# Performance work log

Hardware: AMD Instinct MI355X
Metric: run time of the kernel (lower is better)

Reference implementation:

```python
import jax, jax.numpy as jnp
import numpy as np

N_NODES = 100000
N_EDGES = 1600000
IN_F = 256
OUT_F = 128


def setup_inputs() -> dict:
    key = jax.random.key(0)
    k1, k2, k3, k4, k5, k6 = jax.random.split(key, 6)
    x = jax.random.normal(k1, (N_NODES, IN_F), dtype=jnp.float32)
    edge_row = jax.random.randint(k2, (N_EDGES,), 0, N_NODES)  # destination (output row)
    edge_col = jax.random.randint(k3, (N_EDGES,), 0, N_NODES)  # source (gathered node)
    edge_val = jax.random.uniform(k4, (N_EDGES,), dtype=jnp.float32)  # normalized adj weights
    # Xavier-uniform init like nn.init.xavier_uniform_
    limit = float(np.sqrt(6.0 / (IN_F + OUT_F)))
    weight = jax.random.uniform(k5, (IN_F, OUT_F), dtype=jnp.float32, minval=-limit, maxval=limit)
    bias = jnp.zeros((OUT_F,), dtype=jnp.float32)
    return {"x": x, "edge_row": edge_row, "edge_col": edge_col,
            "edge_val": edge_val, "weight": weight, "bias": bias}


def reference(x, edge_row, edge_col, edge_val, weight, bias):
    # Dense transform: h = x @ W + b   -> [N, OUT_F]
    h = x @ weight + bias
    # Sparse adjacency matmul: out[i] = sum_{e: row[e]==i} val[e] * h[col[e]]
    msg = h[edge_col] * edge_val[:, None]  # [E, OUT_F] gather + scale
    out = jax.ops.segment_sum(msg, edge_row, num_segments=N_NODES)
    return out
```

## Files before the change

kernel.cpp:

```cpp
#include <hip/hip_runtime.h>

#define IN_F 256
#define OUT_F 128

typedef __attribute__((ext_vector_type(8))) short short8;
typedef __attribute__((ext_vector_type(4))) float floatx4;

__device__ __forceinline__ unsigned short f2bf(float f) {
    union { float f; unsigned int u; } v; v.f = f;
    unsigned int u = v.u;
    unsigned int r = (u + 0x7FFFu + ((u >> 16) & 1u)) >> 16;
    return (unsigned short)r;
}

__global__ __launch_bounds__(256) void prep_kernel(
    const float* __restrict__ w, unsigned short* __restrict__ w_t,
    int* __restrict__ ghist, int nb)
{
    const int g = blockIdx.x * 256 + threadIdx.x;
    if (g < IN_F * OUT_F) {
        const int n = g >> 8;
        const int k = g & 255;
        w_t[n * 256 + k] = f2bf(w[k * OUT_F + n]);
    }
    const int z = g - IN_F * OUT_F;
    if (z >= 0 && z < nb) ghist[z] = 0;
}

#define XS2 264
#define HS2 136

__global__ __launch_bounds__(256) void gemm_mfma_kernel(
    const float* __restrict__ x, const unsigned short* __restrict__ w_t,
    const float* __restrict__ bias, unsigned short* __restrict__ h_bf, int M)
{
    __shared__ unsigned short xs[64 * XS2];

    const int tid  = threadIdx.x;
    const int w    = tid >> 6;
    const int l    = tid & 63;
    const int m16  = l & 15;
    const int g    = l >> 4;
    const int row0 = blockIdx.x * 64;

    short8 bf[2][8];
    #pragma unroll
    for (int nt = 0; nt < 2; nt++)
        #pragma unroll
        for (int ks = 0; ks < 8; ks++)
            bf[nt][ks] = *(const short8*)(
                w_t + (w * 32 + nt * 16 + m16) * 256 + ks * 32 + g * 8);

    #pragma unroll
    for (int s = 0; s < 16; s++) {
        const int idx = tid + s * 256;
        const int row = idx >> 6;
        const int c4  = idx & 63;
        const int gr  = row0 + row;
        float4 v = make_float4(0.f, 0.f, 0.f, 0.f);
        if (gr < M) v = *(const float4*)(x + (size_t)gr * IN_F + c4 * 4);
        ushort4 b;
        b.x = f2bf(v.x); b.y = f2bf(v.y); b.z = f2bf(v.z); b.w = f2bf(v.w);
        *(ushort4*)(xs + row * XS2 + c4 * 4) = b;
    }
    __syncthreads();

    floatx4 acc[4][2];
    #pragma unroll
    for (int mt = 0; mt < 4; mt++) {
        acc[mt][0] = (floatx4){0.f, 0.f, 0.f, 0.f};
        acc[mt][1] = (floatx4){0.f, 0.f, 0.f, 0.f};
    }

    #pragma unroll
    for (int ks = 0; ks < 8; ks++) {
        #pragma unroll
        for (int mt = 0; mt < 4; mt++) {
            const short8 a = *(const short8*)(xs + (mt * 16 + m16) * XS2 + ks * 32 + g * 8);
            acc[mt][0] = __builtin_amdgcn_mfma_f32_16x16x32_bf16(a, bf[0][ks], acc[mt][0], 0, 0, 0);
            acc[mt][1] = __builtin_amdgcn_mfma_f32_16x16x32_bf16(a, bf[1][ks], acc[mt][1], 0, 0, 0);
        }
    }
    __syncthreads();

    unsigned short* hs = xs;
    #pragma unroll
    for (int nt = 0; nt < 2; nt++) {
        const int col = w * 32 + nt * 16 + m16;
        const float bv = bias[col];
        #pragma unroll
        for (int mt = 0; mt < 4; mt++)
            #pragma unroll
            for (int r = 0; r < 4; r++)
                hs[(mt * 16 + g * 4 + r) * HS2 + col] = f2bf(acc[mt][nt][r] + bv);
    }
    __syncthreads();

    {
        const int row = tid >> 2;
        const int seg = tid & 3;
        const int gr  = row0 + row;
        if (gr < M) {
            #pragma unroll
            for (int q = 0; q < 4; q++) {
                const uint4 v = *(const uint4*)(hs + row * HS2 + seg * 32 + q * 8);
                *(uint4*)(h_bf + (size_t)gr * OUT_F + seg * 32 + q * 8) = v;
            }
        }
    }
}


__global__ __launch_bounds__(256) void hist_kernel(
    const int* __restrict__ erow, int* __restrict__ ghist, int E, int nb)
{
    __shared__ int lh[512];
    for (int i = threadIdx.x; i < nb; i += 256) lh[i] = 0;
    __syncthreads();
    const int base = blockIdx.x * 8192;
    for (int i = 0; i < 32; i++) {
        const int e = base + i * 256 + threadIdx.x;
        if (e < E) atomicAdd(&lh[erow[e] >> 8], 1);
    }
    __syncthreads();
    for (int i = threadIdx.x; i < nb; i += 256)
        if (lh[i]) atomicAdd(&ghist[i], lh[i]);
}

__global__ __launch_bounds__(512) void scanb_kernel(
    const int* __restrict__ ghist, int* __restrict__ bucketStart,
    int* __restrict__ cursor, int nb, int M, int E, int* __restrict__ start)
{
    __shared__ int sd[512];
    const int t = threadIdx.x;
    const int v = (t < nb) ? ghist[t] : 0;
    sd[t] = v;
    __syncthreads();
    for (int off = 1; off < 512; off <<= 1) {
        const int u = (t >= off) ? sd[t - off] : 0;
        __syncthreads();
        sd[t] += u;
        __syncthreads();
    }
    if (t < nb) { const int ex = sd[t] - v; bucketStart[t] = ex; cursor[t] = ex; }
    if (t == 0) { bucketStart[nb] = E; start[M] = E; }
}

__global__ __launch_bounds__(256) void sort_kernel(
    const int* __restrict__ erow, const int* __restrict__ ecol,
    const float* __restrict__ eval, int* __restrict__ cursor,
    uint2* __restrict__ tmp, int E, int nb)
{
    __shared__ int lcnt[512], lbase[512];
    for (int i = threadIdx.x; i < nb; i += 256) lcnt[i] = 0;
    __syncthreads();
    const int base = blockIdx.x * 8192;
    for (int i = 0; i < 32; i++) {
        const int e = base + i * 256 + threadIdx.x;
        if (e < E) atomicAdd(&lcnt[erow[e] >> 8], 1);
    }
    __syncthreads();
    for (int i = threadIdx.x; i < nb; i += 256) {
        const int c = lcnt[i];
        lbase[i] = c ? atomicAdd(&cursor[i], c) : 0;
        lcnt[i] = 0;
    }
    __syncthreads();
    for (int i = 0; i < 32; i++) {
        const int e = base + i * 256 + threadIdx.x;
        if (e < E) {
            const int r = erow[e];
            const int b = r >> 8;
            const int lp = atomicAdd(&lcnt[b], 1);
            tmp[lbase[b] + lp] = make_uint2(
                ((unsigned int)(r & 255) << 24) | (unsigned int)ecol[e],
                __float_as_uint(eval[e]));
        }
    }
}

__global__ __launch_bounds__(256) void csr_kernel(
    const uint2* __restrict__ tmp, const int* __restrict__ bucketStart,
    int* __restrict__ start, unsigned int* __restrict__ cv, int M)
{
    __shared__ int nh[256], nst[256], ncur[256];
    __shared__ unsigned int lcv[8192];
    const int b  = blockIdx.x;
    const int s0 = bucketStart[b];
    const int s1 = bucketStart[b + 1];
    const int cnt = min(s1 - s0, 8192);
    const int t  = threadIdx.x;

    nh[t] = 0;
    __syncthreads();
    for (int i = t; i < cnt; i += 256) atomicAdd(&nh[tmp[s0 + i].x >> 24], 1);
    __syncthreads();

    const int v = nh[t];
    nst[t] = v;
    __syncthreads();
    for (int off = 1; off < 256; off <<= 1) {
        const int u = (t >= off) ? nst[t - off] : 0;
        __syncthreads();
        nst[t] += u;
        __syncthreads();
    }
    const int ex = nst[t] - v;
    const int node = b * 256 + t;
    if (node < M) start[node] = s0 + ex;
    ncur[t] = ex;
    __syncthreads();

    for (int i = t; i < cnt; i += 256) {
        const uint2 p = tmp[s0 + i];
        const int d  = p.x >> 24;
        const int lp = atomicAdd(&ncur[d], 1);
        const float f = __uint_as_float(p.y);
        const int q = min((int)(f * 32768.0f), 32767);
        lcv[lp] = ((p.x & 0x00FFFFFFu) << 15) | (unsigned int)q;
    }
    __syncthreads();
    for (int i = t; i < cnt; i += 256) cv[s0 + i] = lcv[i];
}

__global__ __launch_bounds__(256) void gather_kernel(
    const unsigned short* __restrict__ h_bf, const int* __restrict__ start,
    const unsigned int* __restrict__ cv, float* __restrict__ out, int N)
{
    const int node = (blockIdx.x * 256 + threadIdx.x) >> 6;
    const int lane = threadIdx.x & 63;
    if (node >= N) return;

    const int s   = start[node];
    const int end = start[node + 1];
    const unsigned int* hp = (const unsigned int*)h_bf;

    float acc0 = 0.f, acc1 = 0.f;
    int j = s;
    for (; j + 8 <= end; j += 8) {
        unsigned int mu[8];
        const unsigned int* rp[8];
        #pragma unroll
        for (int u = 0; u < 8; u++) {
            mu[u] = __builtin_amdgcn_readfirstlane(cv[j + u]);
            rp[u] = hp + (size_t)(mu[u] >> 15) * 64;
        }
        unsigned int p[8];
        #pragma unroll
        for (int u = 0; u < 8; u++) p[u] = rp[u][lane];
        #pragma unroll
        for (int u = 0; u < 8; u++) {
            const float v = (float)(mu[u] & 0x7FFFu) * (1.0f / 32768.0f) + (0.5f / 32768.0f);
            acc0 += v * __uint_as_float(p[u] << 16);
            acc1 += v * __uint_as_float(p[u] & 0xFFFF0000u);
        }
    }
    for (; j < end; j++) {
        const unsigned int mu = __builtin_amdgcn_readfirstlane(cv[j]);
        const unsigned int p = *(hp + (size_t)(mu >> 15) * 64 + lane);
        const float v = (float)(mu & 0x7FFFu) * (1.0f / 32768.0f) + (0.5f / 32768.0f);
        acc0 += v * __uint_as_float(p << 16);
        acc1 += v * __uint_as_float(p & 0xFFFF0000u);
    }
    float2 o; o.x = acc0; o.y = acc1;
    *(float2*)(out + (size_t)node * OUT_F + lane * 2) = o;
}

extern "C" void kernel_launch(void* const* d_in, const int* in_sizes, int n_in,
                              void* d_out, int out_size, void* d_ws, size_t ws_size,
                              hipStream_t stream) {
    const float* x     = (const float*)d_in[0];
    const int*   erow  = (const int*)d_in[1];
    const int*   ecol  = (const int*)d_in[2];
    const float* eval  = (const float*)d_in[3];
    const float* wgt   = (const float*)d_in[4];
    const float* bias  = (const float*)d_in[5];
    float*       out   = (float*)d_out;

    const int M  = in_sizes[0] / IN_F;
    const int E  = in_sizes[1];
    const int nb = (M + 255) >> 8;
    const int EB = (E + 8191) / 8192;

    char* ws = (char*)d_ws;
    unsigned short* h_bf = (unsigned short*)ws;  ws += (size_t)M * OUT_F * 2;
    unsigned short* w_t  = (unsigned short*)ws;  ws += (size_t)IN_F * OUT_F * 2;
    int* ghist       = (int*)ws;                 ws += ((size_t)nb * 4 + 15) & ~15ull;
    int* bucketStart = (int*)ws;                 ws += ((size_t)(nb + 1) * 4 + 15) & ~15ull;
    int* cursor      = (int*)ws;                 ws += ((size_t)nb * 4 + 15) & ~15ull;
    int* start       = (int*)ws;                 ws += ((size_t)(M + 1) * 4 + 15) & ~15ull;
    uint2* tmp       = (uint2*)ws;               ws += (size_t)E * 8;
    unsigned int* cv = (unsigned int*)ws;        ws += (size_t)E * 4;

    prep_kernel<<<(IN_F * OUT_F + nb + 255) / 256, 256, 0, stream>>>(wgt, w_t, ghist, nb);
    gemm_mfma_kernel<<<(M + 63) / 64, 256, 0, stream>>>(x, w_t, bias, h_bf, M);

    hist_kernel<<<EB, 256, 0, stream>>>(erow, ghist, E, nb);
    scanb_kernel<<<1, 512, 0, stream>>>(ghist, bucketStart, cursor, nb, M, E, start);
    sort_kernel<<<EB, 256, 0, stream>>>(erow, ecol, eval, cursor, tmp, E, nb);
    csr_kernel<<<nb, 256, 0, stream>>>(tmp, bucketStart, start, cv, M);

    const long long work = (long long)M * 64;
    gather_kernel<<<(int)((work + 255) / 256), 256, 0, stream>>>(
        h_bf, start, cv, out, M);
}
```

Measured before the change: 339.1 us.

## Split GEMM tiles across hist, sort and CSR kernels to overlap work

The dense GEMM is split into three tile ranges, and each range is fused as extra blocks into the histogram, sort and CSR-build kernels via blockIdx dispatch with shared smem buffers. This lets the compute-bound GEMM run alongside the latency- and atomic-bound CSR construction stages, filling idle CUs and removing the standalone GEMM launch. The cost is that each fused kernel now reserves the larger shared-memory footprint for every block, which can lower occupancy for the small hist and sort blocks. GEMM tiles can also end up scheduled unevenly behind those blocks.

```diff
diff --git a/kernel.cpp b/kernel.cpp
--- a/kernel.cpp
+++ b/kernel.cpp
@@ -29,19 +29,23 @@
 
 #define XS2 264
 #define HS2 136
-
-__global__ __launch_bounds__(256) void gemm_mfma_kernel(
+#define GEMM_SMEM 33792
+#define CSR_SMEM  35840
+
+__device__ __forceinline__ void gemm_body(
+    char* smem,
     const float* __restrict__ x, const unsigned short* __restrict__ w_t,
-    const float* __restrict__ bias, unsigned short* __restrict__ h_bf, int M)
-{
-    __shared__ unsigned short xs[64 * XS2];
+    const float* __restrict__ bias, unsigned short* __restrict__ h_bf,
+    int tile, int M)
+{
+    unsigned short* xs = (unsigned short*)smem;
 
     const int tid  = threadIdx.x;
     const int w    = tid >> 6;
     const int l    = tid & 63;
     const int m16  = l & 15;
     const int g    = l >> 4;
-    const int row0 = blockIdx.x * 64;
+    const int row0 = tile * 64;
 
     short8 bf[2][8];
     #pragma unroll
@@ -110,14 +114,14 @@
     }
 }
 
-
-__global__ __launch_bounds__(256) void hist_kernel(
-    const int* __restrict__ erow, int* __restrict__ ghist, int E, int nb)
-{
-    __shared__ int lh[512];
+__device__ __forceinline__ void hist_body(
+    char* smem, const int* __restrict__ erow, int* __restrict__ ghist,
+    int E, int nb, int blk)
+{
+    int* lh = (int*)smem;
     for (int i = threadIdx.x; i < nb; i += 256) lh[i] = 0;
     __syncthreads();
-    const int base = blockIdx.x * 8192;
+    const int base = blk * 8192;
     for (int i = 0; i < 32; i++) {
         const int e = base + i * 256 + threadIdx.x;
         if (e < E) atomicAdd(&lh[erow[e] >> 8], 1);
@@ -127,34 +131,16 @@
         if (lh[i]) atomicAdd(&ghist[i], lh[i]);
 }
 
-__global__ __launch_bounds__(512) void scanb_kernel(
-    const int* __restrict__ ghist, int* __restrict__ bucketStart,
-    int* __restrict__ cursor, int nb, int M, int E, int* __restrict__ start)
-{
-    __shared__ int sd[512];
-    const int t = threadIdx.x;
-    const int v = (t < nb) ? ghist[t] : 0;
-    sd[t] = v;
-    __syncthreads();
-    for (int off = 1; off < 512; off <<= 1) {
-        const int u = (t >= off) ? sd[t - off] : 0;
-        __syncthreads();
-        sd[t] += u;
-        __syncthreads();
-    }
-    if (t < nb) { const int ex = sd[t] - v; bucketStart[t] = ex; cursor[t] = ex; }
-    if (t == 0) { bucketStart[nb] = E; start[M] = E; }
-}
-
-__global__ __launch_bounds__(256) void sort_kernel(
-    const int* __restrict__ erow, const int* __restrict__ ecol,
+__device__ __forceinline__ void sort_body(
+    char* smem, const int* __restrict__ erow, const int* __restrict__ ecol,
     const float* __restrict__ eval, int* __restrict__ cursor,
-    uint2* __restrict__ tmp, int E, int nb)
-{
-    __shared__ int lcnt[512], lbase[512];
+    uint2* __restrict__ tmp, int E, int nb, int blk)
+{
+    int* lcnt  = (int*)smem;
+    int* lbase = lcnt + 512;
     for (int i = threadIdx.x; i < nb; i += 256) lcnt[i] = 0;
     __syncthreads();
-    const int base = blockIdx.x * 8192;
+    const int base = blk * 8192;
     for (int i = 0; i < 32; i++) {
         const int e = base + i * 256 + threadIdx.x;
         if (e < E) atomicAdd(&lcnt[erow[e] >> 8], 1);
@@ -179,13 +165,16 @@
     }
 }
 
-__global__ __launch_bounds__(256) void csr_kernel(
-    const uint2* __restrict__ tmp, const int* __restrict__ bucketStart,
-    int* __restrict__ start, unsigned int* __restrict__ cv, int M)
-{
-    __shared__ int nh[256], nst[256], ncur[256];
-    __shared__ unsigned int lcv[8192];
-    const int b  = blockIdx.x;
+__device__ __forceinline__ void csr_body(
+    char* smem, const uint2* __restrict__ tmp, const int* __restrict__ bucketStart,
+    int* __restrict__ start, unsigned int* __restrict__ cv, int M, int blk)
+{
+    int* nh   = (int*)smem;
+    int* nst  = nh + 256;
+    int* ncur = nst + 256;
+    unsigned int* lcv = (unsigned int*)(smem + 3072);
+
+    const int b  = blk;
     const int s0 = bucketStart[b];
     const int s1 = bucketStart[b + 1];
     const int cnt = min(s1 - s0, 8192);
@@ -221,6 +210,67 @@
     }
     __syncthreads();
     for (int i = t; i < cnt; i += 256) cv[s0 + i] = lcv[i];
+}
+
+__global__ __launch_bounds__(256) void k_hist_gemm(
+    const int* __restrict__ erow, int* __restrict__ ghist, int E, int nb, int EB,
+    const float* __restrict__ x, const unsigned short* __restrict__ w_t,
+    const float* __restrict__ bias, unsigned short* __restrict__ h_bf,
+    int M, int tile0)
+{
+    __shared__ __align__(16) char smem[GEMM_SMEM];
+    if ((int)blockIdx.x < EB)
+        hist_body(smem, erow, ghist, E, nb, blockIdx.x);
+    else
+        gemm_body(smem, x, w_t, bias, h_bf, tile0 + (int)blockIdx.x - EB, M);
+}
+
+__global__ __launch_bounds__(256) void k_sort_gemm(
+    const int* __restrict__ erow, const int* __restrict__ ecol,
+    const float* __restrict__ eval, int* __restrict__ cursor,
+    uint2* __restrict__ tmp, int E, int nb, int EB,
+    const float* __restrict__ x, const unsigned short* __restrict__ w_t,
+    const float* __restrict__ bias, unsigned short* __restrict__ h_bf,
+    int M, int tile0)
+{
+    __shared__ __align__(16) char smem[GEMM_SMEM];
+    if ((int)blockIdx.x < EB)
+        sort_body(smem, erow, ecol, eval, cursor, tmp, E, nb, blockIdx.x);
+    else
+        gemm_body(smem, x, w_t, bias, h_bf, tile0 + (int)blockIdx.x - EB, M);
+}
+
+__global__ __launch_bounds__(256) void k_csr_gemm(
+    const uint2* __restrict__ tmp, const int* __restrict__ bucketStart,
+    int* __restrict__ start, unsigned int* __restrict__ cv, int nb,
+    const float* __restrict__ x, const unsigned short* __restrict__ w_t,
+    const float* __restrict__ bias, unsigned short* __restrict__ h_bf,
+    int M, int tile0)
+{
+    __shared__ __align__(16) char smem[CSR_SMEM];
+    if ((int)blockIdx.x < nb)
+        csr_body(smem, tmp, bucketStart, start, cv, M, blockIdx.x);
+    else
+        gemm_body(smem, x, w_t, bias, h_bf, tile0 + (int)blockIdx.x - nb, M);
+}
+
+__global__ __launch_bounds__(512) void scanb_kernel(
+    const int* __restrict__ ghist, int* __restrict__ bucketStart,
+    int* __restrict__ cursor, int nb, int M, int E, int* __restrict__ start)
+{
+    __shared__ int sd[512];
+    const int t = threadIdx.x;
+    const int v = (t < nb) ? ghist[t] : 0;
+    sd[t] = v;
+    __syncthreads();
+    for (int off = 1; off < 512; off <<= 1) {
+        const int u = (t >= off) ? sd[t - off] : 0;
+        __syncthreads();
+        sd[t] += u;
+        __syncthreads();
+    }
+    if (t < nb) { const int ex = sd[t] - v; bucketStart[t] = ex; cursor[t] = ex; }
+    if (t == 0) { bucketStart[nb] = E; start[M] = E; }
 }
 
 __global__ __launch_bounds__(256) void gather_kernel(
@@ -281,6 +331,9 @@
     const int E  = in_sizes[1];
     const int nb = (M + 255) >> 8;
     const int EB = (E + 8191) / 8192;
+    const int GT = (M + 63) / 64;
+    const int TA = GT / 3;
+    const int TB = (2 * GT) / 3;
 
     char* ws = (char*)d_ws;
     unsigned short* h_bf = (unsigned short*)ws;  ws += (size_t)M * OUT_F * 2;
@@ -293,12 +346,17 @@
     unsigned int* cv = (unsigned int*)ws;        ws += (size_t)E * 4;
 
     prep_kernel<<<(IN_F * OUT_F + nb + 255) / 256, 256, 0, stream>>>(wgt, w_t, ghist, nb);
-    gemm_mfma_kernel<<<(M + 63) / 64, 256, 0, stream>>>(x, w_t, bias, h_bf, M);
-
-    hist_kernel<<<EB, 256, 0, stream>>>(erow, ghist, E, nb);
+
+    k_hist_gemm<<<EB + TA, 256, 0, stream>>>(erow, ghist, E, nb, EB,
+                                             x, w_t, bias, h_bf, M, 0);
+
     scanb_kernel<<<1, 512, 0, stream>>>(ghist, bucketStart, cursor, nb, M, E, start);
-    sort_kernel<<<EB, 256, 0, stream>>>(erow, ecol, eval, cursor, tmp, E, nb);
-    csr_kernel<<<nb, 256, 0, stream>>>(tmp, bucketStart, start, cv, M);
+
+    k_sort_gemm<<<EB + (TB - TA), 256, 0, stream>>>(erow, ecol, eval, cursor, tmp, E, nb, EB,
+                                                    x, w_t, bias, h_bf, M, TA);
+
+    k_csr_gemm<<<nb + (GT - TB), 256, 0, stream>>>(tmp, bucketStart, start, cv, nb,
+                                                   x, w_t, bias, h_bf, M, TB);
 
     const long long work = (long long)M * 64;
     gather_kernel<<<(int)((work + 255) / 256), 256, 0, stream>>>(
```

After: 326.7 us. 3.6% less time.
